# Kernel optimization log

Measured on AMD Instinct MI355X. Metric: run time of the kernel, lower is better.

The kernel has to match this reference:

```python
import jax, jax.numpy as jnp
import numpy as np

N, E, D, G, FP = 20000, 320000, 1280, 64, 65


def _glorot(k, shape):
    s = jnp.sqrt(6.0 / (shape[0] + shape[1])).astype(jnp.float32)
    return jax.random.uniform(k, shape, jnp.float32, -s, s)


def setup_inputs() -> dict:
    key = jax.random.key(0)
    ks = jax.random.split(key, 16)
    return {
        'x': jax.random.normal(ks[0], (N, D), jnp.float32),
        'edge_index': jax.random.randint(ks[1], (2, E), 0, N),
        'batch': jnp.sort(jax.random.randint(ks[2], (N,), 0, G)),
        'fp_x': jax.random.normal(ks[3], (G, FP), jnp.float32),
        'W1': _glorot(ks[4], (D, D)), 'b1': jnp.zeros((D,), jnp.float32),
        'W2': _glorot(ks[5], (D, 640)), 'b2': jnp.zeros((640,), jnp.float32),
        'W3': _glorot(ks[6], (640, 320)), 'b3': jnp.zeros((320,), jnp.float32),
        'Wg1': _glorot(ks[7], (320, 1024)), 'bg1': jnp.zeros((1024,), jnp.float32),
        'Wg2': _glorot(ks[8], (1024, 128)), 'bg2': jnp.zeros((128,), jnp.float32),
        'Wf1': _glorot(ks[9], (193, 1024)), 'bf1': jnp.zeros((1024,), jnp.float32),
        'Wf2': _glorot(ks[10], (1024, 512)), 'bf2': jnp.zeros((512,), jnp.float32),
        'Wo': _glorot(ks[11], (512, 1)), 'bo': jnp.zeros((1,), jnp.float32),
    }


def reference(x, edge_index, batch, fp_x, W1, b1, W2, b2, W3, b3,
              Wg1, bg1, Wg2, bg2, Wf1, bf1, Wf2, bf2, Wo, bo):
    n = x.shape[0]
    g = fp_x.shape[0]
    loop = jnp.arange(n)
    src = jnp.concatenate([edge_index[0], loop])  # self-loops added (GCNConv default)
    dst = jnp.concatenate([edge_index[1], loop])
    deg = jax.ops.segment_sum(jnp.ones_like(dst, x.dtype), dst, num_segments=n)
    dis = jnp.where(deg > 0, jax.lax.rsqrt(deg), 0.0)
    norm = dis[src] * dis[dst]  # D^-1/2 (A+I) D^-1/2 edge weights

    def gcn(h, W, b):
        h = h @ W                                  # transform first (PyG GCNConv)
        agg = jax.ops.segment_sum(h[src] * norm[:, None], dst, num_segments=n)
        return agg + b

    xt = jax.nn.relu(gcn(x, W1, b1))
    xt = jax.nn.relu(gcn(xt, W2, b2))
    xt = jax.nn.relu(gcn(xt, W3, b3))
    # global mean pool over graphs
    s = jax.ops.segment_sum(xt, batch, num_segments=g)
    cnt = jax.ops.segment_sum(jnp.ones((n,), xt.dtype), batch, num_segments=g)
    xt = s / jnp.maximum(cnt, 1.0)[:, None]
    # MLP head (dropout in eval mode -> identity)
    xt = jax.nn.relu(xt @ Wg1 + bg1)
    xt = xt @ Wg2 + bg2
    xc = jnp.concatenate([fp_x, xt], axis=1)       # [G, 65+128=193]
    xc = jax.nn.relu(xc @ Wf1 + bf1)
    xc = jax.nn.relu(xc @ Wf2 + bf2)
    return xc @ Wo + bo
```

## Files before the change

kernel.cpp:

```cpp
#include <hip/hip_runtime.h>
#include <hip/hip_bf16.h>

#define N_NODES 20000
#define NPAD    20224
#define N_EDGES 320000
#define NGRAPH  64
#define FPD     65

typedef __attribute__((ext_vector_type(8))) __bf16 bf16x8;
typedef __attribute__((ext_vector_type(4))) float floatx4;
typedef __attribute__((ext_vector_type(8))) ushort ushort8v;

__device__ inline float bf2f(ushort u) {
    union { unsigned int i; float f; } c; c.i = ((unsigned int)u) << 16; return c.f;
}
__device__ inline ushort f2bf(float v) {
    __hip_bfloat16 h = __float2bfloat16(v);
    return *(ushort*)&h;
}
__device__ __forceinline__ void gld_lds16(const ushort* g, ushort* l) {
    __builtin_amdgcn_global_load_lds(
        (const __attribute__((address_space(1))) unsigned int*)g,
        (__attribute__((address_space(3))) unsigned int*)l,
        16, 0, 0);
}

__global__ void init_cnt(int* cnt) {
    int i = blockIdx.x * blockDim.x + threadIdx.x;
    if (i < N_NODES) cnt[i] = 1;
}
__global__ void count_in(const int* __restrict__ dst, int* cnt) {
    int e = blockIdx.x * blockDim.x + threadIdx.x;
    if (e < N_EDGES) atomicAdd(&cnt[dst[e]], 1);
}
__global__ __launch_bounds__(256) void scan_offsets(const int* __restrict__ cnt,
                                                    int* __restrict__ off, int* __restrict__ cursor,
                                                    float* __restrict__ dis) {
    __shared__ int part[256];
    int t = threadIdx.x;
    const int chunk = (N_NODES + 255) / 256;
    int lo = t * chunk, hi = min(lo + chunk, N_NODES);
    int s = 0;
    for (int i = lo; i < hi; ++i) s += (cnt[i] + 3) & ~3;
    part[t] = s;
    __syncthreads();
    for (int d = 1; d < 256; d <<= 1) {
        int v = (t >= d) ? part[t - d] : 0;
        __syncthreads();
        part[t] += v;
        __syncthreads();
    }
    int base = part[t] - s;
    for (int i = lo; i < hi; ++i) {
        int c = cnt[i];
        off[i] = base; cursor[i] = base;
        dis[i] = rsqrtf((float)c);
        base += (c + 3) & ~3;
    }
    if (t == 255) off[N_NODES] = part[255];
}
__global__ void fill_csr(const int* __restrict__ src, const int* __restrict__ dst,
                         const float* __restrict__ dis, int* cursor,
                         int* __restrict__ esrc, float* __restrict__ ew) {
    int e = blockIdx.x * blockDim.x + threadIdx.x;
    if (e >= N_EDGES + N_NODES) return;
    int s, d; float w;
    if (e < N_EDGES) { s = src[e]; d = dst[e]; w = dis[s] * dis[d]; }
    else { s = d = e - N_EDGES; w = dis[s] * dis[s]; }
    int pos = atomicAdd(&cursor[d], 1);
    esrc[pos] = s; ew[pos] = w;
}
__global__ void fill_pad(const int* __restrict__ off, const int* __restrict__ cursor,
                         int* __restrict__ esrc, float* __restrict__ ew) {
    int i = blockIdx.x * blockDim.x + threadIdx.x;
    if (i >= N_NODES) return;
    int e1 = off[i + 1];
    for (int e = cursor[i]; e < e1; ++e) { esrc[e] = i; ew[e] = 0.f; }
}

__global__ void conv_f32_bf16_tiled(const float* __restrict__ in, ushort* __restrict__ out) {
    int idx = blockIdx.x * blockDim.x + threadIdx.x;
    if (idx >= N_NODES * 320) return;
    int n = idx / 320, f4 = idx % 320;
    float4 v = *(const float4*)(in + (size_t)n * 1280 + f4 * 4);
    ushort4 o;
    o.x = f2bf(v.x); o.y = f2bf(v.y); o.z = f2bf(v.z); o.w = f2bf(v.w);
    *(ushort4*)(out + (size_t)(f4 >> 4) * (NPAD * 64) + (size_t)n * 64 + (f4 & 15) * 4) = o;
}
__global__ void transpose_conv(const float* __restrict__ W, ushort* __restrict__ Wt,
                               int K, int Nc, int KP) {
    __shared__ float t[32][33];
    int k0 = blockIdx.x * 32, n0 = blockIdx.y * 32;
    int tx = threadIdx.x, ty = threadIdx.y;
    #pragma unroll
    for (int i = 0; i < 4; ++i)
        t[ty + i * 8][tx] = W[(size_t)(k0 + ty + i * 8) * Nc + n0 + tx];
    __syncthreads();
    #pragma unroll
    for (int i = 0; i < 4; ++i)
        Wt[(size_t)(n0 + ty + i * 8) * KP + k0 + tx] = f2bf(t[tx][ty + i * 8]);
}

__global__ __launch_bounds__(256) void gemm_bf16_128(
    const ushort* __restrict__ A, const ushort* __restrict__ Bt,
    ushort* __restrict__ C, int M, int K, int KP, int Nc, int nt, int total, int chunk)
{
    __shared__ ushort As[128 * 64];
    __shared__ ushort Bs[128 * 64];
    const int bi = blockIdx.x;
    const int tile = (bi & 7) * chunk + (bi >> 3);
    if (tile >= total) return;
    const int bm = (tile / nt) * 128, bn = (tile % nt) * 128;

    const int tid = threadIdx.x;
    const int wid = tid >> 6, lane = tid & 63;
    const int wr = wid >> 1, wc = wid & 1;
    const int quad = lane >> 4, mr = lane & 15;

    floatx4 acc[4][4];
    #pragma unroll
    for (int i = 0; i < 4; ++i)
        #pragma unroll
        for (int j = 0; j < 4; ++j)
            acc[i][j] = (floatx4){0.f, 0.f, 0.f, 0.f};

    for (int k0 = 0; k0 < K; k0 += 64) {
        const ushort* Ak = A + (size_t)(k0 >> 6) * (NPAD * 64);
        #pragma unroll
        for (int i = 0; i < 4; ++i) {
            int c = tid + i * 256;
            int row = c >> 3, g = c & 7;
            gld_lds16(Ak + (size_t)(bm + row) * 64 + (g ^ (row & 7)) * 8, &As[c * 8]);
        }
        #pragma unroll
        for (int i = 0; i < 4; ++i) {
            int c = tid + i * 256;
            int row = c >> 3, g = c & 7;
            gld_lds16(Bt + (size_t)(bn + row) * KP + k0 + (g ^ (row & 7)) * 8, &Bs[c * 8]);
        }
        __syncthreads();

        #pragma unroll
        for (int ks = 0; ks < 2; ++ks) {
            bf16x8 af[4], bfv[4];
            #pragma unroll
            for (int t = 0; t < 4; ++t) {
                int ra = wr * 64 + t * 16 + mr;
                af[t] = *(const bf16x8*)&As[ra * 64 + ((ks * 4 + quad) ^ (ra & 7)) * 8];
                int rb = wc * 64 + t * 16 + mr;
                bfv[t] = *(const bf16x8*)&Bs[rb * 64 + ((ks * 4 + quad) ^ (rb & 7)) * 8];
            }
            #pragma unroll
            for (int tm = 0; tm < 4; ++tm)
                #pragma unroll
                for (int tn = 0; tn < 4; ++tn)
                    acc[tm][tn] = __builtin_amdgcn_mfma_f32_16x16x32_bf16(af[tm], bfv[tn], acc[tm][tn], 0, 0, 0);
        }
        __syncthreads();
    }

    ushort* Cc = C + (size_t)((bn >> 6) + wc) * (NPAD * 64);
    #pragma unroll
    for (int tm = 0; tm < 4; ++tm) {
        int rowb = bm + wr * 64 + tm * 16 + quad * 4;
        #pragma unroll
        for (int r = 0; r < 4; ++r) {
            int row = rowb + r;
            if (row < M) {
                #pragma unroll
                for (int tn = 0; tn < 4; ++tn)
                    Cc[(size_t)row * 64 + tn * 16 + mr] = f2bf(acc[tm][tn][r]);
            }
        }
    }
}

__global__ __launch_bounds__(256) void gemm_bf16(
    const ushort* __restrict__ A, const ushort* __restrict__ Bt,
    ushort* __restrict__ C, int M, int K, int KP, int Nc, int nt, int total, int chunk)
{
    __shared__ ushort As[256 * 64];
    __shared__ ushort Bs[64 * 64];
    const int bi = blockIdx.x;
    const int tile = (bi & 7) * chunk + (bi >> 3);
    if (tile >= total) return;
    const int bm = (tile / nt) * 256, bn = (tile % nt) * 64;

    const int tid = threadIdx.x;
    const int wid = tid >> 6, lane = tid & 63;
    const int quad = lane >> 4, mr = lane & 15;

    floatx4 acc[4][4];
    #pragma unroll
    for (int i = 0; i < 4; ++i)
        #pragma unroll
        for (int j = 0; j < 4; ++j)
            acc[i][j] = (floatx4){0.f, 0.f, 0.f, 0.f};

    for (int k0 = 0; k0 < K; k0 += 64) {
        const ushort* Ak = A + (size_t)(k0 >> 6) * (NPAD * 64);
        #pragma unroll
        for (int i = 0; i < 8; ++i) {
            int c = tid + i * 256;
            int row = c >> 3, g = c & 7;
            gld_lds16(Ak + (size_t)(bm + row) * 64 + (g ^ (row & 7)) * 8, &As[c * 8]);
        }
        #pragma unroll
        for (int i = 0; i < 2; ++i) {
            int c = tid + i * 256;
            int row = c >> 3, g = c & 7;
            gld_lds16(Bt + (size_t)(bn + row) * KP + k0 + (g ^ (row & 7)) * 8, &Bs[c * 8]);
        }
        __syncthreads();

        #pragma unroll
        for (int ks = 0; ks < 2; ++ks) {
            bf16x8 af[4], bfv[4];
            #pragma unroll
            for (int t = 0; t < 4; ++t) {
                int ra = wid * 64 + t * 16 + mr;
                af[t] = *(const bf16x8*)&As[ra * 64 + ((ks * 4 + quad) ^ (ra & 7)) * 8];
                int rb = t * 16 + mr;
                bfv[t] = *(const bf16x8*)&Bs[rb * 64 + ((ks * 4 + quad) ^ (rb & 7)) * 8];
            }
            #pragma unroll
            for (int tm = 0; tm < 4; ++tm)
                #pragma unroll
                for (int tn = 0; tn < 4; ++tn)
                    acc[tm][tn] = __builtin_amdgcn_mfma_f32_16x16x32_bf16(af[tm], bfv[tn], acc[tm][tn], 0, 0, 0);
        }
        __syncthreads();
    }

    ushort* Cc = C + (size_t)(bn >> 6) * (NPAD * 64);
    #pragma unroll
    for (int tm = 0; tm < 4; ++tm) {
        int rowb = bm + wid * 64 + tm * 16 + quad * 4;
        #pragma unroll
        for (int r = 0; r < 4; ++r) {
            int row = rowb + r;
            if (row < M) {
                #pragma unroll
                for (int tn = 0; tn < 4; ++tn)
                    Cc[(size_t)row * 64 + tn * 16 + mr] = f2bf(acc[tm][tn][r]);
            }
        }
    }
}

static inline void launch_gemm(const ushort* A, const ushort* Bt, ushort* C,
                               int M, int K, int KP, int Nc, hipStream_t stream) {
    if (Nc % 128 == 0) {
        int mt = (M + 127) / 128, nt = Nc / 128;
        int total = mt * nt;
        int chunk = (total + 7) / 8;
        gemm_bf16_128<<<8 * chunk, 256, 0, stream>>>(A, Bt, C, M, K, KP, Nc, nt, total, chunk);
    } else {
        int mt = (M + 255) / 256, nt = Nc / 64;
        int total = mt * nt;
        int chunk = (total + 7) / 8;
        gemm_bf16<<<8 * chunk, 256, 0, stream>>>(A, Bt, C, M, K, KP, Nc, nt, total, chunk);
    }
}

template<int TPN>
__global__ __launch_bounds__(256) void gather_tiled(
    const ushort* __restrict__ h, const int* __restrict__ off,
    const int* __restrict__ esrc, const float* __restrict__ ew,
    const float* __restrict__ bias, ushort* __restrict__ out_bf,
    float* __restrict__ out_f32, int wbf, int wf32, int nchunks, int nbpc)
{
    constexpr int NPB = 256 / TPN;
    const int bi = blockIdx.x;
    const int xcd = bi & 7;
    const int t2 = bi >> 3;
    const int s = t2 / nbpc, nb = t2 - s * nbpc;
    const int c = s * 8 + xcd;
    if (c >= nchunks) return;
    const int tid = threadIdx.x;
    const int g = tid / TPN, t = tid % TPN;
    const int n = nb * NPB + g;
    if (n >= N_NODES) return;

    const ushort* hc = h + (size_t)c * (NPAD * 64) + t * 8;
    float acc[8];
    #pragma unroll
    for (int j = 0; j < 8; ++j) acc[j] = 0.f;

    const int e0 = off[n], e1 = off[n + 1];
    for (int e = e0; e < e1; e += 4) {
        int4   s4 = *(const int4*)(esrc + e);
        float4 w4 = *(const float4*)(ew + e);
        ushort8v v0 = *(const ushort8v*)(hc + (size_t)s4.x * 64);
        ushort8v v1 = *(const ushort8v*)(hc + (size_t)s4.y * 64);
        ushort8v v2 = *(const ushort8v*)(hc + (size_t)s4.z * 64);
        ushort8v v3 = *(const ushort8v*)(hc + (size_t)s4.w * 64);
        #pragma unroll
        for (int j = 0; j < 8; ++j)
            acc[j] += w4.x * bf2f(v0[j]) + w4.y * bf2f(v1[j])
                    + w4.z * bf2f(v2[j]) + w4.w * bf2f(v3[j]);
    }

    const int fb = c * 64 + t * 8;
    float4 b0 = *(const float4*)(bias + fb);
    float4 b1 = *(const float4*)(bias + fb + 4);
    float r[8];
    r[0] = fmaxf(acc[0] + b0.x, 0.f); r[1] = fmaxf(acc[1] + b0.y, 0.f);
    r[2] = fmaxf(acc[2] + b0.z, 0.f); r[3] = fmaxf(acc[3] + b0.w, 0.f);
    r[4] = fmaxf(acc[4] + b1.x, 0.f); r[5] = fmaxf(acc[5] + b1.y, 0.f);
    r[6] = fmaxf(acc[6] + b1.z, 0.f); r[7] = fmaxf(acc[7] + b1.w, 0.f);
    if (wbf) {
        ushort8v o;
        #pragma unroll
        for (int j = 0; j < 8; ++j) o[j] = f2bf(r[j]);
        *(ushort8v*)(out_bf + (size_t)c * (NPAD * 64) + (size_t)n * 64 + t * 8) = o;
    }
    if (wf32) {
        *(float4*)(out_f32 + (size_t)n * (nchunks * 64) + fb)     = make_float4(r[0], r[1], r[2], r[3]);
        *(float4*)(out_f32 + (size_t)n * (nchunks * 64) + fb + 4) = make_float4(r[4], r[5], r[6], r[7]);
    }
}

static inline void launch_gather(const ushort* h, const int* off, const int* esrc,
                                 const float* ew, const float* bias, ushort* out_bf,
                                 float* out_f32, int wbf, int wf32, int nchunks,
                                 hipStream_t stream) {
    constexpr int TPN = 8;
    constexpr int NPB = 256 / TPN;
    const int nbpc = (N_NODES + NPB - 1) / NPB;
    const int sblocks = (nchunks + 7) / 8;
    gather_tiled<TPN><<<8 * sblocks * nbpc, 256, 0, stream>>>(
        h, off, esrc, ew, bias, out_bf, out_f32, wbf, wf32, nchunks, nbpc);
}

__global__ void graph_bounds(const int* __restrict__ batch, int* __restrict__ gstart) {
    int n = blockIdx.x * blockDim.x + threadIdx.x;
    if (n >= N_NODES) return;
    int b = batch[n];
    int bp = (n == 0) ? -1 : batch[n - 1];
    for (int g = bp + 1; g <= b; ++g) gstart[g] = n;
    if (n == N_NODES - 1)
        for (int g = b + 1; g <= NGRAPH; ++g) gstart[g] = N_NODES;
}
__global__ __launch_bounds__(320) void pool_graph(
    const float* __restrict__ x, const int* __restrict__ gstart, float* __restrict__ pool)
{
    int g = blockIdx.x;
    int t = threadIdx.x;
    int s = gstart[g], e = gstart[g + 1];
    float a0 = 0.f, a1 = 0.f, a2 = 0.f, a3 = 0.f;
    int n = s;
    for (; n + 3 < e; n += 4) {
        a0 += x[(size_t)(n + 0) * 320 + t];
        a1 += x[(size_t)(n + 1) * 320 + t];
        a2 += x[(size_t)(n + 2) * 320 + t];
        a3 += x[(size_t)(n + 3) * 320 + t];
    }
    for (; n < e; ++n) a0 += x[(size_t)n * 320 + t];
    float acc = (a0 + a1) + (a2 + a3);
    pool[g * 320 + t] = acc / fmaxf((float)(e - s), 1.0f);
}

template<int K, int SPLIT, int RELU>
__global__ __launch_bounds__(256) void head_gemm_sk(
    const float* __restrict__ in, int istride,
    const float* __restrict__ W, const float* __restrict__ b,
    float* __restrict__ out, int M, int Nc)
{
    constexpr int KQ = K / SPLIT;
    int idx = blockIdx.x * blockDim.x + threadIdx.x;
    int oi = idx / SPLIT, r = idx % SPLIT;
    if (oi >= M * Nc) return;
    int m = oi / Nc, c = oi % Nc;
    const float* ip = in + (size_t)m * istride + r * KQ;
    const float* wp = W + (size_t)r * KQ * Nc + c;
    float a0 = 0.f, a1 = 0.f, a2 = 0.f, a3 = 0.f;
    #pragma unroll
    for (int k = 0; k < KQ; k += 4) {
        float4 v = *(const float4*)(ip + k);
        a0 += v.x * wp[(size_t)(k + 0) * Nc];
        a1 += v.y * wp[(size_t)(k + 1) * Nc];
        a2 += v.z * wp[(size_t)(k + 2) * Nc];
        a3 += v.w * wp[(size_t)(k + 3) * Nc];
    }
    float s = (a0 + a1) + (a2 + a3);
    #pragma unroll
    for (int o = 1; o < SPLIT; o <<= 1) s += __shfl_xor(s, o, 64);
    if (r == 0) {
        s += b[c];
        out[oi] = RELU ? fmaxf(s, 0.f) : s;
    }
}

__global__ void head_prep(const float* __restrict__ fp, const float* __restrict__ xt,
                          float* __restrict__ xc, const float* __restrict__ Wf1,
                          float* __restrict__ Wp) {
    int idx = blockIdx.x * blockDim.x + threadIdx.x;
    if (idx < 208 * 1024) {
        int k = idx / 1024;
        Wp[idx] = (k < 193) ? Wf1[idx] : 0.f;
    }
    if (idx < NGRAPH * 208) {
        int g = idx / 208, j = idx % 208;
        float v = 0.f;
        if (j < FPD) v = fp[g * FPD + j];
        else if (j < 193) v = xt[g * 128 + (j - FPD)];
        xc[idx] = v;
    }
}

__global__ __launch_bounds__(256) void head_out(
    const float* __restrict__ f2, const float* __restrict__ Wo,
    const float* __restrict__ bo, float* __restrict__ out)
{
    int m = blockIdx.x;
    int t = threadIdx.x;
    float2 v = *(const float2*)(f2 + (size_t)m * 512 + t * 2);
    float2 w = *(const float2*)(Wo + t * 2);
    float s = v.x * w.x + v.y * w.y;
    #pragma unroll
    for (int o = 32; o > 0; o >>= 1) s += __shfl_down(s, o, 64);
    __shared__ float ps[4];
    if ((t & 63) == 0) ps[t >> 6] = s;
    __syncthreads();
    if (t == 0) out[m] = ps[0] + ps[1] + ps[2] + ps[3] + bo[0];
}

extern "C" void kernel_launch(void* const* d_in, const int* in_sizes, int n_in,
                              void* d_out, int out_size, void* d_ws, size_t ws_size,
                              hipStream_t stream) {
    const float* x    = (const float*)d_in[0];
    const int*   eidx = (const int*)d_in[1];
    const int*   batch= (const int*)d_in[2];
    const float* fp_x = (const float*)d_in[3];
    const float* W1 = (const float*)d_in[4];  const float* b1 = (const float*)d_in[5];
    const float* W2 = (const float*)d_in[6];  const float* b2 = (const float*)d_in[7];
    const float* W3 = (const float*)d_in[8];  const float* b3 = (const float*)d_in[9];
    const float* Wg1= (const float*)d_in[10]; const float* bg1= (const float*)d_in[11];
    const float* Wg2= (const float*)d_in[12]; const float* bg2= (const float*)d_in[13];
    const float* Wf1= (const float*)d_in[14]; const float* bf1= (const float*)d_in[15];
    const float* Wf2= (const float*)d_in[16]; const float* bf2= (const float*)d_in[17];
    const float* Wo = (const float*)d_in[18]; const float* bo = (const float*)d_in[19];
    float* out = (float*)d_out;

    const int* src = eidx;
    const int* dst = eidx + N_EDGES;

    char* p = (char*)d_ws;
    float* dis   = (float*)p;  p += 20480 * 4;
    int*   cntI  = (int*)p;    p += 20480 * 4;
    int*   off   = (int*)p;    p += 20480 * 4;
    int*   cursor= (int*)p;    p += 20480 * 4;
    int*   gstart= (int*)p;    p += 128 * 4;
    int*   esrc  = (int*)p;    p += 402432 * 4;
    float* ew    = (float*)p;  p += 402432 * 4;
    ushort* xbf  = (ushort*)p; p += (size_t)NPAD * 1280 * 2;
    ushort* hbf  = (ushort*)p; p += (size_t)NPAD * 1280 * 2;
    ushort* abf  = (ushort*)p; p += (size_t)NPAD * 1280 * 2;
    float* a3f   = (float*)p;  p += (size_t)N_NODES * 320 * 4;
    ushort* Wt   = (ushort*)p; p += (size_t)1280 * 1344 * 2;
    float* pool  = (float*)p;  p += NGRAPH * 320 * 4;
    float* m1    = (float*)p;  p += NGRAPH * 1024 * 4;
    float* m2    = (float*)p;  p += NGRAPH * 128 * 4;
    float* xc    = (float*)p;  p += NGRAPH * 208 * 4;
    float* f1    = (float*)p;  p += NGRAPH * 1024 * 4;
    float* f2    = (float*)p;  p += NGRAPH * 512 * 4;
    float* Wf1p  = (float*)p;  p += 208 * 1024 * 4;

    init_cnt<<<(N_NODES + 255) / 256, 256, 0, stream>>>(cntI);
    count_in<<<(N_EDGES + 255) / 256, 256, 0, stream>>>(dst, cntI);
    scan_offsets<<<1, 256, 0, stream>>>(cntI, off, cursor, dis);
    fill_csr<<<(N_EDGES + N_NODES + 255) / 256, 256, 0, stream>>>(src, dst, dis, cursor, esrc, ew);
    fill_pad<<<(N_NODES + 255) / 256, 256, 0, stream>>>(off, cursor, esrc, ew);
    graph_bounds<<<(N_NODES + 255) / 256, 256, 0, stream>>>(batch, gstart);

    {
        conv_f32_bf16_tiled<<<(N_NODES * 320 + 255) / 256, 256, 0, stream>>>(x, xbf);
        transpose_conv<<<dim3(1280 / 32, 1280 / 32), dim3(32, 8), 0, stream>>>(W1, Wt, 1280, 1280, 1344);
        launch_gemm(xbf, Wt, hbf, N_NODES, 1280, 1344, 1280, stream);
        launch_gather(hbf, off, esrc, ew, b1, abf, (float*)nullptr, 1, 0, 20, stream);
    }
    {
        transpose_conv<<<dim3(1280 / 32, 640 / 32), dim3(32, 8), 0, stream>>>(W2, Wt, 1280, 640, 1344);
        launch_gemm(abf, Wt, hbf, N_NODES, 1280, 1344, 640, stream);
        launch_gather(hbf, off, esrc, ew, b2, abf, (float*)nullptr, 1, 0, 10, stream);
    }
    {
        transpose_conv<<<dim3(640 / 32, 320 / 32), dim3(32, 8), 0, stream>>>(W3, Wt, 640, 320, 704);
        launch_gemm(abf, Wt, hbf, N_NODES, 640, 704, 320, stream);
        launch_gather(hbf, off, esrc, ew, b3, (ushort*)nullptr, a3f, 0, 1, 5, stream);
    }

    pool_graph<<<NGRAPH, 320, 0, stream>>>(a3f, gstart, pool);

    head_gemm_sk<320, 4, 1><<<(NGRAPH * 1024 * 4 + 255) / 256, 256, 0, stream>>>(pool, 320, Wg1, bg1, m1, NGRAPH, 1024);
    head_gemm_sk<1024, 8, 0><<<(NGRAPH * 128 * 8 + 255) / 256, 256, 0, stream>>>(m1, 1024, Wg2, bg2, m2, NGRAPH, 128);
    head_prep<<<(208 * 1024 + 255) / 256, 256, 0, stream>>>(fp_x, m2, xc, Wf1, Wf1p);
    head_gemm_sk<208, 4, 1><<<(NGRAPH * 1024 * 4 + 255) / 256, 256, 0, stream>>>(xc, 208, Wf1p, bf1, f1, NGRAPH, 1024);
    head_gemm_sk<1024, 8, 1><<<(NGRAPH * 512 * 8 + 255) / 256, 256, 0, stream>>>(f1, 1024, Wf2, bf2, f2, NGRAPH, 512);
    head_out<<<NGRAPH, 256, 0, stream>>>(f2, Wo, bo, out);
}
```

Baseline: 724.5 us.

## Double-buffer LDS tiles in bf16 GEMMs and widen offset scan to 1024 threads

Both GEMM kernels now keep two LDS buffers per operand and issue the async global-to-LDS loads for the next K tile before computing on the current one. This removes one barrier per K step and is meant to overlap memory latency with MFMA work. The cost is double the LDS footprint (64 KB for the 128x128 kernel and 80 KB for the 256x64 kernel), which can lower occupancy. Separately, the single-block offset scan uses 1024 threads instead of 256, which shortens each thread's serial chunk.

Result: faster. 700.4 us (-3.3%).

```diff
diff --git a/kernel.cpp b/kernel.cpp
--- a/kernel.cpp
+++ b/kernel.cpp
@@ -33,18 +33,18 @@
     int e = blockIdx.x * blockDim.x + threadIdx.x;
     if (e < N_EDGES) atomicAdd(&cnt[dst[e]], 1);
 }
-__global__ __launch_bounds__(256) void scan_offsets(const int* __restrict__ cnt,
-                                                    int* __restrict__ off, int* __restrict__ cursor,
-                                                    float* __restrict__ dis) {
-    __shared__ int part[256];
+__global__ __launch_bounds__(1024) void scan_offsets(const int* __restrict__ cnt,
+                                                     int* __restrict__ off, int* __restrict__ cursor,
+                                                     float* __restrict__ dis) {
+    __shared__ int part[1024];
     int t = threadIdx.x;
-    const int chunk = (N_NODES + 255) / 256;
+    const int chunk = (N_NODES + 1023) / 1024;
     int lo = t * chunk, hi = min(lo + chunk, N_NODES);
     int s = 0;
     for (int i = lo; i < hi; ++i) s += (cnt[i] + 3) & ~3;
     part[t] = s;
     __syncthreads();
-    for (int d = 1; d < 256; d <<= 1) {
+    for (int d = 1; d < 1024; d <<= 1) {
         int v = (t >= d) ? part[t - d] : 0;
         __syncthreads();
         part[t] += v;
@@ -57,7 +57,7 @@
         dis[i] = rsqrtf((float)c);
         base += (c + 3) & ~3;
     }
-    if (t == 255) off[N_NODES] = part[255];
+    if (t == 1023) off[N_NODES] = part[1023];
 }
 __global__ void fill_csr(const int* __restrict__ src, const int* __restrict__ dst,
                          const float* __restrict__ dis, int* cursor,
@@ -101,12 +101,49 @@
         Wt[(size_t)(n0 + ty + i * 8) * KP + k0 + tx] = f2bf(t[tx][ty + i * 8]);
 }
 
+
+#define STAGE128(AsB, BsB, kt) do {                                                   \
+    const ushort* Ak_ = A + (size_t)(kt) * (NPAD * 64);                               \
+    const ushort* Bk_ = Bt + (size_t)(kt) * 64;                                       \
+    _Pragma("unroll")                                                                 \
+    for (int i_ = 0; i_ < 4; ++i_) {                                                  \
+        int c_ = tid + i_ * 256;                                                      \
+        int row_ = c_ >> 3, g_ = c_ & 7;                                              \
+        gld_lds16(Ak_ + (size_t)(bm + row_) * 64 + (g_ ^ (row_ & 7)) * 8, &AsB[c_ * 8]); \
+    }                                                                                 \
+    _Pragma("unroll")                                                                 \
+    for (int i_ = 0; i_ < 4; ++i_) {                                                  \
+        int c_ = tid + i_ * 256;                                                      \
+        int row_ = c_ >> 3, g_ = c_ & 7;                                              \
+        gld_lds16(Bk_ + (size_t)(bn + row_) * KP + (g_ ^ (row_ & 7)) * 8, &BsB[c_ * 8]); \
+    }                                                                                 \
+} while (0)
+
+#define COMPUTE128(AsB, BsB) do {                                                     \
+    _Pragma("unroll")                                                                 \
+    for (int ks = 0; ks < 2; ++ks) {                                                  \
+        bf16x8 af[4], bfv[4];                                                         \
+        _Pragma("unroll")                                                             \
+        for (int t = 0; t < 4; ++t) {                                                 \
+            int ra = wr * 64 + t * 16 + mr;                                           \
+            af[t] = *(const bf16x8*)&AsB[ra * 64 + ((ks * 4 + quad) ^ (ra & 7)) * 8]; \
+            int rb = wc * 64 + t * 16 + mr;                                           \
+            bfv[t] = *(const bf16x8*)&BsB[rb * 64 + ((ks * 4 + quad) ^ (rb & 7)) * 8];\
+        }                                                                             \
+        _Pragma("unroll")                                                             \
+        for (int tm = 0; tm < 4; ++tm)                                                \
+            _Pragma("unroll")                                                         \
+            for (int tn = 0; tn < 4; ++tn)                                            \
+                acc[tm][tn] = __builtin_amdgcn_mfma_f32_16x16x32_bf16(af[tm], bfv[tn], acc[tm][tn], 0, 0, 0); \
+    }                                                                                 \
+} while (0)
+
 __global__ __launch_bounds__(256) void gemm_bf16_128(
     const ushort* __restrict__ A, const ushort* __restrict__ Bt,
     ushort* __restrict__ C, int M, int K, int KP, int Nc, int nt, int total, int chunk)
 {
-    __shared__ ushort As[128 * 64];
-    __shared__ ushort Bs[128 * 64];
+    __shared__ ushort As0[128 * 64], As1[128 * 64];
+    __shared__ ushort Bs0[128 * 64], Bs1[128 * 64];
     const int bi = blockIdx.x;
     const int tile = (bi & 7) * chunk + (bi >> 3);
     if (tile >= total) return;
@@ -124,39 +161,18 @@
         for (int j = 0; j < 4; ++j)
             acc[i][j] = (floatx4){0.f, 0.f, 0.f, 0.f};
 
-    for (int k0 = 0; k0 < K; k0 += 64) {
-        const ushort* Ak = A + (size_t)(k0 >> 6) * (NPAD * 64);
-        #pragma unroll
-        for (int i = 0; i < 4; ++i) {
-            int c = tid + i * 256;
-            int row = c >> 3, g = c & 7;
-            gld_lds16(Ak + (size_t)(bm + row) * 64 + (g ^ (row & 7)) * 8, &As[c * 8]);
+    const int NT = K >> 6;
+    STAGE128(As0, Bs0, 0);
+    __syncthreads();
+    for (int kt = 0; kt < NT; kt += 2) {
+        if (kt + 1 < NT) STAGE128(As1, Bs1, kt + 1);
+        COMPUTE128(As0, Bs0);
+        __syncthreads();
+        if (kt + 1 < NT) {
+            if (kt + 2 < NT) STAGE128(As0, Bs0, kt + 2);
+            COMPUTE128(As1, Bs1);
+            __syncthreads();
         }
-        #pragma unroll
-        for (int i = 0; i < 4; ++i) {
-            int c = tid + i * 256;
-            int row = c >> 3, g = c & 7;
-            gld_lds16(Bt + (size_t)(bn + row) * KP + k0 + (g ^ (row & 7)) * 8, &Bs[c * 8]);
-        }
-        __syncthreads();
-
-        #pragma unroll
-        for (int ks = 0; ks < 2; ++ks) {
-            bf16x8 af[4], bfv[4];
-            #pragma unroll
-            for (int t = 0; t < 4; ++t) {
-                int ra = wr * 64 + t * 16 + mr;
-                af[t] = *(const bf16x8*)&As[ra * 64 + ((ks * 4 + quad) ^ (ra & 7)) * 8];
-                int rb = wc * 64 + t * 16 + mr;
-                bfv[t] = *(const bf16x8*)&Bs[rb * 64 + ((ks * 4 + quad) ^ (rb & 7)) * 8];
-            }
-            #pragma unroll
-            for (int tm = 0; tm < 4; ++tm)
-                #pragma unroll
-                for (int tn = 0; tn < 4; ++tn)
-                    acc[tm][tn] = __builtin_amdgcn_mfma_f32_16x16x32_bf16(af[tm], bfv[tn], acc[tm][tn], 0, 0, 0);
-        }
-        __syncthreads();
     }
 
     ushort* Cc = C + (size_t)((bn >> 6) + wc) * (NPAD * 64);
@@ -175,12 +191,48 @@
     }
 }
 
+#define STAGE64(AsB, BsB, kt) do {                                                    \
+    const ushort* Ak_ = A + (size_t)(kt) * (NPAD * 64);                               \
+    const ushort* Bk_ = Bt + (size_t)(kt) * 64;                                       \
+    _Pragma("unroll")                                                                 \
+    for (int i_ = 0; i_ < 8; ++i_) {                                                  \
+        int c_ = tid + i_ * 256;                                                      \
+        int row_ = c_ >> 3, g_ = c_ & 7;                                              \
+        gld_lds16(Ak_ + (size_t)(bm + row_) * 64 + (g_ ^ (row_ & 7)) * 8, &AsB[c_ * 8]); \
+    }                                                                                 \
+    _Pragma("unroll")                                                                 \
+    for (int i_ = 0; i_ < 2; ++i_) {                                                  \
+        int c_ = tid + i_ * 256;                                                      \
+        int row_ = c_ >> 3, g_ = c_ & 7;                                              \
+        gld_lds16(Bk_ + (size_t)(bn + row_) * KP + (g_ ^ (row_ & 7)) * 8, &BsB[c_ * 8]); \
+    }                                                                                 \
+} while (0)
+
+#define COMPUTE64(AsB, BsB) do {                                                      \
+    _Pragma("unroll")                                                                 \
+    for (int ks = 0; ks < 2; ++ks) {                                                  \
+        bf16x8 af[4], bfv[4];                                                         \
+        _Pragma("unroll")                                                             \
+        for (int t = 0; t < 4; ++t) {                                                 \
+            int ra = wid * 64 + t * 16 + mr;                                          \
+            af[t] = *(const bf16x8*)&AsB[ra * 64 + ((ks * 4 + quad) ^ (ra & 7)) * 8]; \
+            int rb = t * 16 + mr;                                                     \
+            bfv[t] = *(const bf16x8*)&BsB[rb * 64 + ((ks * 4 + quad) ^ (rb & 7)) * 8];\
+        }                                                                             \
+        _Pragma("unroll")                                                             \
+        for (int tm = 0; tm < 4; ++tm)                                                \
+            _Pragma("unroll")                                                         \
+            for (int tn = 0; tn < 4; ++tn)                                            \
+                acc[tm][tn] = __builtin_amdgcn_mfma_f32_16x16x32_bf16(af[tm], bfv[tn], acc[tm][tn], 0, 0, 0); \
+    }                                                                                 \
+} while (0)
+
 __global__ __launch_bounds__(256) void gemm_bf16(
     const ushort* __restrict__ A, const ushort* __restrict__ Bt,
     ushort* __restrict__ C, int M, int K, int KP, int Nc, int nt, int total, int chunk)
 {
-    __shared__ ushort As[256 * 64];
-    __shared__ ushort Bs[64 * 64];
+    __shared__ ushort As0[256 * 64], As1[256 * 64];
+    __shared__ ushort Bs0[64 * 64], Bs1[64 * 64];
     const int bi = blockIdx.x;
     const int tile = (bi & 7) * chunk + (bi >> 3);
     if (tile >= total) return;
@@ -197,39 +249,18 @@
         for (int j = 0; j < 4; ++j)
             acc[i][j] = (floatx4){0.f, 0.f, 0.f, 0.f};
 
-    for (int k0 = 0; k0 < K; k0 += 64) {
-        const ushort* Ak = A + (size_t)(k0 >> 6) * (NPAD * 64);
-        #pragma unroll
-        for (int i = 0; i < 8; ++i) {
-            int c = tid + i * 256;
-            int row = c >> 3, g = c & 7;
-            gld_lds16(Ak + (size_t)(bm + row) * 64 + (g ^ (row & 7)) * 8, &As[c * 8]);
+    const int NT = K >> 6;
+    STAGE64(As0, Bs0, 0);
+    __syncthreads();
+    for (int kt = 0; kt < NT; kt += 2) {
+        if (kt + 1 < NT) STAGE64(As1, Bs1, kt + 1);
+        COMPUTE64(As0, Bs0);
+        __syncthreads();
+        if (kt + 1 < NT) {
+            if (kt + 2 < NT) STAGE64(As0, Bs0, kt + 2);
+            COMPUTE64(As1, Bs1);
+            __syncthreads();
         }
-        #pragma unroll
-        for (int i = 0; i < 2; ++i) {
-            int c = tid + i * 256;
-            int row = c >> 3, g = c & 7;
-            gld_lds16(Bt + (size_t)(bn + row) * KP + k0 + (g ^ (row & 7)) * 8, &Bs[c * 8]);
-        }
-        __syncthreads();
-
-        #pragma unroll
-        for (int ks = 0; ks < 2; ++ks) {
-            bf16x8 af[4], bfv[4];
-            #pragma unroll
-            for (int t = 0; t < 4; ++t) {
-                int ra = wid * 64 + t * 16 + mr;
-                af[t] = *(const bf16x8*)&As[ra * 64 + ((ks * 4 + quad) ^ (ra & 7)) * 8];
-                int rb = t * 16 + mr;
-                bfv[t] = *(const bf16x8*)&Bs[rb * 64 + ((ks * 4 + quad) ^ (rb & 7)) * 8];
-            }
-            #pragma unroll
-            for (int tm = 0; tm < 4; ++tm)
-                #pragma unroll
-                for (int tn = 0; tn < 4; ++tn)
-                    acc[tm][tn] = __builtin_amdgcn_mfma_f32_16x16x32_bf16(af[tm], bfv[tn], acc[tm][tn], 0, 0, 0);
-        }
-        __syncthreads();
     }
 
     ushort* Cc = C + (size_t)(bn >> 6) * (NPAD * 64);
@@ -469,7 +500,7 @@
 
     init_cnt<<<(N_NODES + 255) / 256, 256, 0, stream>>>(cntI);
     count_in<<<(N_EDGES + 255) / 256, 256, 0, stream>>>(dst, cntI);
-    scan_offsets<<<1, 256, 0, stream>>>(cntI, off, cursor, dis);
+    scan_offsets<<<1, 1024, 0, stream>>>(cntI, off, cursor, dis);
     fill_csr<<<(N_EDGES + N_NODES + 255) / 256, 256, 0, stream>>>(src, dst, dis, cursor, esrc, ew);
     fill_pad<<<(N_NODES + 255) / 256, 256, 0, stream>>>(off, cursor, esrc, ew);
     graph_bounds<<<(N_NODES + 255) / 256, 256, 0, stream>>>(batch, gstart);
```
